# Performance work log

Hardware: AMD Instinct MI355X
Metric: run time of the kernel (lower is better)

## Reference

```python
import jax, jax.numpy as jnp
import numpy as np

N = 100000      # nodes
E = 1600000     # directed edges
F_IN = 128      # node feature dim
H = 128         # hidden dim
C = 16          # classes


def setup_inputs() -> dict:
    key = jax.random.key(0)
    ks = jax.random.split(key, 8)
    s = 1.0 / np.sqrt(H)
    return {
        "x": jax.random.normal(ks[0], (N, F_IN), dtype=jnp.float32),
        "edge_index": jax.random.randint(ks[1], (2, E), 0, N, dtype=jnp.int32),
        "W1": jax.random.normal(ks[2], (F_IN, H), dtype=jnp.float32) * s,
        "b1": jnp.zeros((H,), jnp.float32),
        "W2": jax.random.normal(ks[3], (H, H), dtype=jnp.float32) * s,
        "b2": jnp.zeros((H,), jnp.float32),
        "W3": jax.random.normal(ks[4], (H, H), dtype=jnp.float32) * s,
        "b3": jnp.zeros((H,), jnp.float32),
        "Wfc": jax.random.normal(ks[5], (H, C), dtype=jnp.float32) * s,
        "bfc": jnp.zeros((C,), jnp.float32),
    }


def _gcn_conv(x, W, b, src, dst, norm):
    # x' = b + scatter_add over edges of norm * (x @ W)[src] into dst
    h = x @ W                                   # [N, H] dense GEMM
    msg = h[src] * norm[:, None]                # [E+N, H] gather + scale
    out = jax.ops.segment_sum(msg, dst, num_segments=N)  # scatter-add
    return out + b


def reference(x, edge_index, W1, b1, W2, b2, W3, b3, Wfc, bfc):
    loops = jnp.arange(N, dtype=edge_index.dtype)
    src = jnp.concatenate([edge_index[0], loops])   # [E+N] with self-loops
    dst = jnp.concatenate([edge_index[1], loops])
    # symmetric normalization deg^{-1/2}[src] * deg^{-1/2}[dst] (PyG default)
    deg = jax.ops.segment_sum(jnp.ones_like(dst, dtype=x.dtype), dst, num_segments=N)
    dinv = jax.lax.rsqrt(deg)                       # deg >= 1 due to self-loops
    norm = dinv[src] * dinv[dst]

    h = jax.nn.elu(_gcn_conv(x, W1, b1, src, dst, norm))   # dropout is identity in eval
    h = jax.nn.elu(_gcn_conv(h, W2, b2, src, dst, norm))
    h = jax.nn.elu(_gcn_conv(h, W3, b3, src, dst, norm))
    logits = h @ Wfc + bfc                                  # [N, C]
    return jax.nn.log_softmax(logits, axis=-1)
```

## Files before the change

### kernel.cpp

```cpp
#include <hip/hip_runtime.h>
#include <math.h>

#define HDIM 128
#define CDIM 16
#define CAP 48
#define ASTR 136
#define NBINS 256
#define TILE 4096

typedef unsigned short u16;
typedef unsigned int u32;
typedef __attribute__((ext_vector_type(8))) short short8;
typedef __attribute__((ext_vector_type(4))) float f32x4;

__device__ inline u16 f2bf(float f) {
  u32 u = __float_as_uint(f);
  u += 0x7fffu + ((u >> 16) & 1u);
  return (u16)(u >> 16);
}
__device__ inline float bf_lo(u32 p) { return __uint_as_float(p << 16); }
__device__ inline float bf_hi(u32 p) { return __uint_as_float(p & 0xffff0000u); }
__device__ inline u32 pack2(float a, float b) {
  return (u32)f2bf(a) | ((u32)f2bf(b) << 16);
}
__device__ inline void addp(float2* a, uint4 g) {
  float2 p0 = make_float2(bf_lo(g.x), bf_hi(g.x));
  float2 p1 = make_float2(bf_lo(g.y), bf_hi(g.y));
  float2 p2 = make_float2(bf_lo(g.z), bf_hi(g.z));
  float2 p3 = make_float2(bf_lo(g.w), bf_hi(g.w));
  a[0].x += p0.x; a[0].y += p0.y;
  a[1].x += p1.x; a[1].y += p1.y;
  a[2].x += p2.x; a[2].y += p2.y;
  a[3].x += p3.x; a[3].y += p3.y;
}


__global__ __launch_bounds__(256) void bin_kernel(const int* __restrict__ ei,
                                                  int* __restrict__ cursor,
                                                  int2* __restrict__ bins,
                                                  int binCap, int E, int npb) {
  __shared__ int2 eds[TILE];
  __shared__ int base[NBINS], rank[NBINS], hist[NBINS];
  int tid = threadIdx.x;
  int t0 = blockIdx.x * TILE;
  int n = min(TILE, E - t0);
  for (int i = tid; i < NBINS; i += 256) { hist[i] = 0; rank[i] = 0; }
  __syncthreads();
  for (int i = tid; i < n; i += 256) {
    int s = ei[t0 + i];
    int d = ei[E + t0 + i];
    eds[i] = make_int2(d, s);
    atomicAdd(&hist[d / npb], 1);
  }
  __syncthreads();
  for (int i = tid; i < NBINS; i += 256) {
    int h = hist[i];
    base[i] = h ? atomicAdd(&cursor[i], h) : 0;
  }
  __syncthreads();
  for (int i = tid; i < n; i += 256) {
    int2 e = eds[i];
    int b = e.x / npb;
    int r = base[b] + atomicAdd(&rank[b], 1);
    if (r < binCap) bins[(size_t)b * binCap + r] = e;
  }
}

__global__ __launch_bounds__(256) void fill2_kernel(const int2* __restrict__ bins,
                                                    const int* __restrict__ cursor,
                                                    int binCap, int* __restrict__ deg,
                                                    int* __restrict__ csr,
                                                    float* __restrict__ dinv, int npb, int N) {
  int b = blockIdx.x;
  int cnt = min(cursor[b], binCap);
  const int2* eb = bins + (size_t)b * binCap;
  for (int i = threadIdx.x; i < cnt; i += 256) {
    int2 e = eb[i];
    int p = atomicAdd(&deg[e.x], 1);
    if (p < CAP) csr[(size_t)e.x * CAP + p] = e.y;
  }
  __syncthreads();
  int lo = b * npb, hi = min(lo + npb, N);
  for (int i = lo + threadIdx.x; i < hi; i += 256)
    dinv[i] = rsqrtf((float)(deg[i] + 1));
}


__global__ void prep_kernel(const float* __restrict__ W0, const float* __restrict__ W1,
                            const float* __restrict__ W2, u16* __restrict__ Wt) {
  int t = blockIdx.x * 256 + threadIdx.x;
  int which = t >> 14, idx = t & 16383;
  int n = idx >> 7, k = idx & 127;
  const float* W = which == 0 ? W0 : (which == 1 ? W1 : W2);
  Wt[(size_t)which * HDIM * HDIM + n * HDIM + k] = f2bf(W[k * HDIM + n]);
}


template <bool FP32IN>
__global__ __launch_bounds__(256) void gemm_k(const void* __restrict__ Xv,
                                              const u16* __restrict__ Wt,
                                              const float* __restrict__ dinv,
                                              u16* __restrict__ G, int N) {
  __shared__ u16 As[64 * ASTR];
  __shared__ u16 Wsm[128 * ASTR];
  int tid = threadIdx.x;
  int row0 = blockIdx.x * 64;

  {
    int r = tid >> 2, c = tid & 3;
    int rg = row0 + r;
    if (rg >= N) rg = N - 1;
    uint4* dst = (uint4*)(As + r * ASTR + c * 32);
    if (FP32IN) {
      const float4* src = (const float4*)((const float*)Xv + (size_t)rg * HDIM + c * 32);
#pragma unroll
      for (int j = 0; j < 4; ++j) {
        float4 a = src[2 * j], b = src[2 * j + 1];
        uint4 o;
        o.x = pack2(a.x, a.y); o.y = pack2(a.z, a.w);
        o.z = pack2(b.x, b.y); o.w = pack2(b.z, b.w);
        dst[j] = o;
      }
    } else {
      const uint4* src = (const uint4*)((const u16*)Xv + (size_t)rg * HDIM + c * 32);
      dst[0] = src[0]; dst[1] = src[1]; dst[2] = src[2]; dst[3] = src[3];
    }
  }
  {
    int r = tid >> 1, h = tid & 1;
    const uint4* src = (const uint4*)(Wt + r * HDIM + h * 64);
    uint4* dst = (uint4*)(Wsm + r * ASTR + h * 64);
#pragma unroll
    for (int i = 0; i < 8; ++i) dst[i] = src[i];
  }
  __syncthreads();

  int w = tid >> 6;
  int l = tid & 63;
  int m = l & 15, q = l >> 4;

  f32x4 acc[8];
#pragma unroll
  for (int i = 0; i < 8; ++i) acc[i] = (f32x4){0.f, 0.f, 0.f, 0.f};

#pragma unroll
  for (int kc = 0; kc < 4; ++kc) {
    short8 af = *(const short8*)(As + (w * 16 + m) * ASTR + kc * 32 + q * 8);
#pragma unroll
    for (int nt = 0; nt < 8; ++nt) {
      short8 bfr = *(const short8*)(Wsm + (nt * 16 + m) * ASTR + kc * 32 + q * 8);
      acc[nt] = __builtin_amdgcn_mfma_f32_16x16x32_bf16(af, bfr, acc[nt], 0, 0, 0);
    }
  }
  __syncthreads();

  float dv[4];
#pragma unroll
  for (int r = 0; r < 4; ++r) {
    int rg = row0 + w * 16 + q * 4 + r;
    dv[r] = dinv[rg < N ? rg : N - 1];
  }
#pragma unroll
  for (int nt = 0; nt < 8; ++nt)
#pragma unroll
    for (int r = 0; r < 4; ++r)
      As[(w * 16 + q * 4 + r) * ASTR + nt * 16 + m] = f2bf(acc[nt][r] * dv[r]);
  __syncthreads();

  {
    int r = tid >> 2, c = tid & 3;
    int rg = row0 + r;
    if (rg < N) {
      uint4* dst = (uint4*)(G + (size_t)rg * HDIM + c * 32);
      const uint4* src = (const uint4*)(As + r * ASTR + c * 32);
      dst[0] = src[0]; dst[1] = src[1]; dst[2] = src[2]; dst[3] = src[3];
    }
  }
}


__device__ inline void gather_node(const u16* __restrict__ G, const int* __restrict__ deg,
                                   const int* __restrict__ csr, const float* __restrict__ dinv,
                                   const float4* __restrict__ b4, int node, int l, float* v) {
  float2 a[4];
  {
    uint4 s = *(const uint4*)(G + (size_t)node * HDIM + l * 8);
    a[0] = make_float2(bf_lo(s.x), bf_hi(s.x));
    a[1] = make_float2(bf_lo(s.y), bf_hi(s.y));
    a[2] = make_float2(bf_lo(s.z), bf_hi(s.z));
    a[3] = make_float2(bf_lo(s.w), bf_hi(s.w));
  }
  int d = min(deg[node], CAP);
  const int* row = csr + (size_t)node * CAP;
  int i = 0;
  for (; i + 4 <= d; i += 4) {
    int u0 = row[i], u1 = row[i + 1], u2 = row[i + 2], u3 = row[i + 3];
    uint4 g0 = *(const uint4*)(G + (size_t)u0 * HDIM + l * 8);
    uint4 g1 = *(const uint4*)(G + (size_t)u1 * HDIM + l * 8);
    uint4 g2 = *(const uint4*)(G + (size_t)u2 * HDIM + l * 8);
    uint4 g3 = *(const uint4*)(G + (size_t)u3 * HDIM + l * 8);
    addp(a, g0); addp(a, g1); addp(a, g2); addp(a, g3);
  }
  for (; i < d; ++i) {
    uint4 g = *(const uint4*)(G + (size_t)row[i] * HDIM + l * 8);
    addp(a, g);
  }
  float dvn = dinv[node];
  float4 b0 = b4[l * 2], b1 = b4[l * 2 + 1];
  v[0] = fmaf(dvn, a[0].x, b0.x); v[1] = fmaf(dvn, a[0].y, b0.y);
  v[2] = fmaf(dvn, a[1].x, b0.z); v[3] = fmaf(dvn, a[1].y, b0.w);
  v[4] = fmaf(dvn, a[2].x, b1.x); v[5] = fmaf(dvn, a[2].y, b1.y);
  v[6] = fmaf(dvn, a[3].x, b1.z); v[7] = fmaf(dvn, a[3].y, b1.w);
#pragma unroll
  for (int j = 0; j < 8; ++j) v[j] = v[j] > 0.f ? v[j] : expm1f(v[j]);
}


__global__ __launch_bounds__(256) void agg_bf(const u16* __restrict__ G,
                                              const int* __restrict__ deg,
                                              const int* __restrict__ csr,
                                              const float* __restrict__ dinv,
                                              const float* __restrict__ b,
                                              u16* __restrict__ out, int N) {
  int node = blockIdx.x * 16 + (threadIdx.x >> 4);
  if (node >= N) return;
  int l = threadIdx.x & 15;
  float v[8];
  gather_node(G, deg, csr, dinv, (const float4*)b, node, l, v);
  uint4 o;
  o.x = pack2(v[0], v[1]); o.y = pack2(v[2], v[3]);
  o.z = pack2(v[4], v[5]); o.w = pack2(v[6], v[7]);
  *(uint4*)(out + (size_t)node * HDIM + l * 8) = o;
}


__global__ __launch_bounds__(256) void agg_fc(const u16* __restrict__ G,
                                              const int* __restrict__ deg,
                                              const int* __restrict__ csr,
                                              const float* __restrict__ dinv,
                                              const float* __restrict__ b,
                                              const float* __restrict__ Wfc,
                                              const float* __restrict__ bfc,
                                              float* __restrict__ out, int N) {
  __shared__ u16 As[16 * ASTR];
  __shared__ float Wl[HDIM * CDIM];
  int tid = threadIdx.x;
  for (int i = tid; i < HDIM * CDIM; i += 256) Wl[i] = Wfc[i];

  int node0 = blockIdx.x * 16;
  int lr = tid >> 4, l = tid & 15;
  int node = node0 + lr;
  if (node < N) {
    float v[8];
    gather_node(G, deg, csr, dinv, (const float4*)b, node, l, v);
    uint4 o;
    o.x = pack2(v[0], v[1]); o.y = pack2(v[2], v[3]);
    o.z = pack2(v[4], v[5]); o.w = pack2(v[6], v[7]);
    *(uint4*)(As + lr * ASTR + l * 8) = o;
  }
  __syncthreads();

  int rg = node0 + lr;
  if (rg >= N) return;
  int c = l;
  const u16* hrow = As + lr * ASTR;
  float acc = bfc[c];
#pragma unroll 4
  for (int k8 = 0; k8 < 16; ++k8) {
    uint4 g = *(const uint4*)(hrow + k8 * 8);
    const float* wk = Wl + (k8 * 8) * CDIM + c;
    acc = fmaf(bf_lo(g.x), wk[0 * CDIM], acc);
    acc = fmaf(bf_hi(g.x), wk[1 * CDIM], acc);
    acc = fmaf(bf_lo(g.y), wk[2 * CDIM], acc);
    acc = fmaf(bf_hi(g.y), wk[3 * CDIM], acc);
    acc = fmaf(bf_lo(g.z), wk[4 * CDIM], acc);
    acc = fmaf(bf_hi(g.z), wk[5 * CDIM], acc);
    acc = fmaf(bf_lo(g.w), wk[6 * CDIM], acc);
    acc = fmaf(bf_hi(g.w), wk[7 * CDIM], acc);
  }
  float mx = acc;
  for (int off = 8; off >= 1; off >>= 1) mx = fmaxf(mx, __shfl_xor(mx, off, 16));
  float ex = expf(acc - mx);
  float ssum = ex;
  for (int off = 8; off >= 1; off >>= 1) ssum += __shfl_xor(ssum, off, 16);
  out[(size_t)rg * CDIM + c] = (acc - mx) - logf(ssum);
}


extern "C" void kernel_launch(void* const* d_in, const int* in_sizes, int n_in,
                              void* d_out, int out_size, void* d_ws, size_t ws_size,
                              hipStream_t stream) {
  const float* x   = (const float*)d_in[0];
  const int*   ei  = (const int*)d_in[1];
  const float* W1  = (const float*)d_in[2];
  const float* b1  = (const float*)d_in[3];
  const float* W2  = (const float*)d_in[4];
  const float* b2  = (const float*)d_in[5];
  const float* W3  = (const float*)d_in[6];
  const float* b3  = (const float*)d_in[7];
  const float* Wfc = (const float*)d_in[8];
  const float* bfc = (const float*)d_in[9];

  const int N = in_sizes[0] / HDIM;
  const int E = in_sizes[1] / 2;
  const int npb = (N + NBINS - 1) / NBINS;
  const int binCap = (E + NBINS - 1) / NBINS + 1024;

  char* ws = (char*)d_ws;
  size_t off = 0;
  auto alloc = [&](size_t bytes) -> void* {
    void* p = ws + off;
    off += (bytes + 511) & ~(size_t)511;
    return p;
  };
  size_t degBytes = ((size_t)N * 4 + 511) & ~(size_t)511;
  int*   deg    = (int*)alloc((size_t)N * 4);
  int*   cursor = (int*)alloc((size_t)NBINS * 4);
  float* dinv   = (float*)alloc((size_t)N * 4);
  int*   csr    = (int*)alloc((size_t)N * CAP * 4);
  int2*  bins   = (int2*)alloc((size_t)NBINS * binCap * 8);
  u16*   Wt     = (u16*)alloc((size_t)3 * HDIM * HDIM * 2);
  u16*   A      = (u16*)alloc((size_t)N * HDIM * 2);
  u16*   B      = (u16*)alloc((size_t)N * HDIM * 2);

  hipMemsetAsync(deg, 0, degBytes + 1024, stream);
  bin_kernel<<<(E + TILE - 1) / TILE, 256, 0, stream>>>(ei, cursor, bins, binCap, E, npb);
  fill2_kernel<<<NBINS, 256, 0, stream>>>(bins, cursor, binCap, deg, csr, dinv, npb, N);
  prep_kernel<<<3 * HDIM * HDIM / 256, 256, 0, stream>>>(W1, W2, W3, Wt);

  int grid64 = (N + 63) / 64;
  int grid16 = (N + 15) / 16;
  gemm_k<true><<<grid64, 256, 0, stream>>>(x, Wt, dinv, A, N);
  agg_bf<<<grid16, 256, 0, stream>>>(A, deg, csr, dinv, b1, B, N);
  gemm_k<false><<<grid64, 256, 0, stream>>>(B, Wt + HDIM * HDIM, dinv, A, N);
  agg_bf<<<grid16, 256, 0, stream>>>(A, deg, csr, dinv, b2, B, N);
  gemm_k<false><<<grid64, 256, 0, stream>>>(B, Wt + 2 * HDIM * HDIM, dinv, A, N);
  agg_fc<<<grid16, 256, 0, stream>>>(A, deg, csr, dinv, b3, Wfc, bfc, (float*)d_out, N);
}
```

Before: 420.2 us.

## Fold weight prep and degree zeroing into binning; split CSR fill; compute dinv inline

The weight transpose and bf16 conversion now run as extra blocks of the binning kernel, which also zeroes the degree array, replacing a separate prep launch and a larger memset. The CSR fill kernel is split four ways per bin so more blocks work in parallel. The dinv array is removed and rsqrt(deg+1) is computed where it is used in the GEMM and aggregation kernels. This cuts kernel launches and the serial tail of the fill step, at the cost of a few extra rsqrt ops and relying on the edge blocks covering all N nodes for zeroing deg.

After: 416.2 us. Within noise of the previous version (-0.9%).

```diff
diff --git a/kernel.cpp b/kernel.cpp
--- a/kernel.cpp
+++ b/kernel.cpp
@@ -7,6 +7,7 @@
 #define ASTR 136
 #define NBINS 256
 #define TILE 4096
+#define F2SPLIT 4
 
 typedef unsigned short u16;
 typedef unsigned int u32;
@@ -24,24 +25,37 @@
   return (u32)f2bf(a) | ((u32)f2bf(b) << 16);
 }
 __device__ inline void addp(float2* a, uint4 g) {
-  float2 p0 = make_float2(bf_lo(g.x), bf_hi(g.x));
-  float2 p1 = make_float2(bf_lo(g.y), bf_hi(g.y));
-  float2 p2 = make_float2(bf_lo(g.z), bf_hi(g.z));
-  float2 p3 = make_float2(bf_lo(g.w), bf_hi(g.w));
-  a[0].x += p0.x; a[0].y += p0.y;
-  a[1].x += p1.x; a[1].y += p1.y;
-  a[2].x += p2.x; a[2].y += p2.y;
-  a[3].x += p3.x; a[3].y += p3.y;
+  a[0].x += bf_lo(g.x); a[0].y += bf_hi(g.x);
+  a[1].x += bf_lo(g.y); a[1].y += bf_hi(g.y);
+  a[2].x += bf_lo(g.z); a[2].y += bf_hi(g.z);
+  a[3].x += bf_lo(g.w); a[3].y += bf_hi(g.w);
 }
 
 
 __global__ __launch_bounds__(256) void bin_kernel(const int* __restrict__ ei,
                                                   int* __restrict__ cursor,
                                                   int2* __restrict__ bins,
-                                                  int binCap, int E, int npb) {
+                                                  int binCap, int E, int npb, int nbE,
+                                                  int* __restrict__ deg, int N,
+                                                  const float* __restrict__ W0,
+                                                  const float* __restrict__ W1,
+                                                  const float* __restrict__ W2,
+                                                  u16* __restrict__ Wt) {
+  int tid = threadIdx.x;
+  if (blockIdx.x >= nbE) {
+    int t = (blockIdx.x - nbE) * 256 + tid;
+    int which = t >> 14, idx = t & 16383;
+    int n = idx >> 7, k = idx & 127;
+    const float* W = which == 0 ? W0 : (which == 1 ? W1 : W2);
+    Wt[(size_t)which * HDIM * HDIM + n * HDIM + k] = f2bf(W[k * HDIM + n]);
+    return;
+  }
+  {
+    int i = blockIdx.x * 256 + tid;
+    if (i < N) deg[i] = 0;
+  }
   __shared__ int2 eds[TILE];
   __shared__ int base[NBINS], rank[NBINS], hist[NBINS];
-  int tid = threadIdx.x;
   int t0 = blockIdx.x * TILE;
   int n = min(TILE, E - t0);
   for (int i = tid; i < NBINS; i += 256) { hist[i] = 0; rank[i] = 0; }
@@ -69,37 +83,23 @@
 __global__ __launch_bounds__(256) void fill2_kernel(const int2* __restrict__ bins,
                                                     const int* __restrict__ cursor,
                                                     int binCap, int* __restrict__ deg,
-                                                    int* __restrict__ csr,
-                                                    float* __restrict__ dinv, int npb, int N) {
-  int b = blockIdx.x;
+                                                    int* __restrict__ csr) {
+  int b = blockIdx.x & (NBINS - 1);
+  int part = blockIdx.x >> 8;
   int cnt = min(cursor[b], binCap);
   const int2* eb = bins + (size_t)b * binCap;
-  for (int i = threadIdx.x; i < cnt; i += 256) {
+  for (int i = part * 256 + threadIdx.x; i < cnt; i += 256 * F2SPLIT) {
     int2 e = eb[i];
     int p = atomicAdd(&deg[e.x], 1);
     if (p < CAP) csr[(size_t)e.x * CAP + p] = e.y;
   }
-  __syncthreads();
-  int lo = b * npb, hi = min(lo + npb, N);
-  for (int i = lo + threadIdx.x; i < hi; i += 256)
-    dinv[i] = rsqrtf((float)(deg[i] + 1));
-}
-
-
-__global__ void prep_kernel(const float* __restrict__ W0, const float* __restrict__ W1,
-                            const float* __restrict__ W2, u16* __restrict__ Wt) {
-  int t = blockIdx.x * 256 + threadIdx.x;
-  int which = t >> 14, idx = t & 16383;
-  int n = idx >> 7, k = idx & 127;
-  const float* W = which == 0 ? W0 : (which == 1 ? W1 : W2);
-  Wt[(size_t)which * HDIM * HDIM + n * HDIM + k] = f2bf(W[k * HDIM + n]);
 }
 
 
 template <bool FP32IN>
 __global__ __launch_bounds__(256) void gemm_k(const void* __restrict__ Xv,
                                               const u16* __restrict__ Wt,
-                                              const float* __restrict__ dinv,
+                                              const int* __restrict__ deg,
                                               u16* __restrict__ G, int N) {
   __shared__ u16 As[64 * ASTR];
   __shared__ u16 Wsm[128 * ASTR];
@@ -158,7 +158,7 @@
 #pragma unroll
   for (int r = 0; r < 4; ++r) {
     int rg = row0 + w * 16 + q * 4 + r;
-    dv[r] = dinv[rg < N ? rg : N - 1];
+    dv[r] = rsqrtf((float)(deg[rg < N ? rg : N - 1] + 1));
   }
 #pragma unroll
   for (int nt = 0; nt < 8; ++nt)
@@ -180,7 +180,7 @@
 
 
 __device__ inline void gather_node(const u16* __restrict__ G, const int* __restrict__ deg,
-                                   const int* __restrict__ csr, const float* __restrict__ dinv,
+                                   const int* __restrict__ csr,
                                    const float4* __restrict__ b4, int node, int l, float* v) {
   float2 a[4];
   {
@@ -190,7 +190,8 @@
     a[2] = make_float2(bf_lo(s.z), bf_hi(s.z));
     a[3] = make_float2(bf_lo(s.w), bf_hi(s.w));
   }
-  int d = min(deg[node], CAP);
+  int dfull = deg[node];
+  int d = min(dfull, CAP);
   const int* row = csr + (size_t)node * CAP;
   int i = 0;
   for (; i + 4 <= d; i += 4) {
@@ -205,7 +206,7 @@
     uint4 g = *(const uint4*)(G + (size_t)row[i] * HDIM + l * 8);
     addp(a, g);
   }
-  float dvn = dinv[node];
+  float dvn = rsqrtf((float)(dfull + 1));
   float4 b0 = b4[l * 2], b1 = b4[l * 2 + 1];
   v[0] = fmaf(dvn, a[0].x, b0.x); v[1] = fmaf(dvn, a[0].y, b0.y);
   v[2] = fmaf(dvn, a[1].x, b0.z); v[3] = fmaf(dvn, a[1].y, b0.w);
@@ -219,14 +220,13 @@
 __global__ __launch_bounds__(256) void agg_bf(const u16* __restrict__ G,
                                               const int* __restrict__ deg,
                                               const int* __restrict__ csr,
-                                              const float* __restrict__ dinv,
                                               const float* __restrict__ b,
                                               u16* __restrict__ out, int N) {
   int node = blockIdx.x * 16 + (threadIdx.x >> 4);
   if (node >= N) return;
   int l = threadIdx.x & 15;
   float v[8];
-  gather_node(G, deg, csr, dinv, (const float4*)b, node, l, v);
+  gather_node(G, deg, csr, (const float4*)b, node, l, v);
   uint4 o;
   o.x = pack2(v[0], v[1]); o.y = pack2(v[2], v[3]);
   o.z = pack2(v[4], v[5]); o.w = pack2(v[6], v[7]);
@@ -237,7 +237,6 @@
 __global__ __launch_bounds__(256) void agg_fc(const u16* __restrict__ G,
                                               const int* __restrict__ deg,
                                               const int* __restrict__ csr,
-                                              const float* __restrict__ dinv,
                                               const float* __restrict__ b,
                                               const float* __restrict__ Wfc,
                                               const float* __restrict__ bfc,
@@ -252,7 +251,7 @@
   int node = node0 + lr;
   if (node < N) {
     float v[8];
-    gather_node(G, deg, csr, dinv, (const float4*)b, node, l, v);
+    gather_node(G, deg, csr, (const float4*)b, node, l, v);
     uint4 o;
     o.x = pack2(v[0], v[1]); o.y = pack2(v[2], v[3]);
     o.z = pack2(v[4], v[5]); o.w = pack2(v[6], v[7]);
@@ -305,6 +304,8 @@
   const int E = in_sizes[1] / 2;
   const int npb = (N + NBINS - 1) / NBINS;
   const int binCap = (E + NBINS - 1) / NBINS + 1024;
+  const int nbE = (E + TILE - 1) / TILE;
+  const int nbW = 3 * HDIM * HDIM / 256;
 
   char* ws = (char*)d_ws;
   size_t off = 0;
@@ -313,27 +314,25 @@
     off += (bytes + 511) & ~(size_t)511;
     return p;
   };
-  size_t degBytes = ((size_t)N * 4 + 511) & ~(size_t)511;
   int*   deg    = (int*)alloc((size_t)N * 4);
   int*   cursor = (int*)alloc((size_t)NBINS * 4);
-  float* dinv   = (float*)alloc((size_t)N * 4);
   int*   csr    = (int*)alloc((size_t)N * CAP * 4);
   int2*  bins   = (int2*)alloc((size_t)NBINS * binCap * 8);
   u16*   Wt     = (u16*)alloc((size_t)3 * HDIM * HDIM * 2);
   u16*   A      = (u16*)alloc((size_t)N * HDIM * 2);
   u16*   B      = (u16*)alloc((size_t)N * HDIM * 2);
 
-  hipMemsetAsync(deg, 0, degBytes + 1024, stream);
-  bin_kernel<<<(E + TILE - 1) / TILE, 256, 0, stream>>>(ei, cursor, bins, binCap, E, npb);
-  fill2_kernel<<<NBINS, 256, 0, stream>>>(bins, cursor, binCap, deg, csr, dinv, npb, N);
-  prep_kernel<<<3 * HDIM * HDIM / 256, 256, 0, stream>>>(W1, W2, W3, Wt);
+  hipMemsetAsync(cursor, 0, (size_t)NBINS * 4, stream);
+  bin_kernel<<<nbE + nbW, 256, 0, stream>>>(ei, cursor, bins, binCap, E, npb, nbE, deg, N, W1,
+                                            W2, W3, Wt);
+  fill2_kernel<<<NBINS * F2SPLIT, 256, 0, stream>>>(bins, cursor, binCap, deg, csr);
 
   int grid64 = (N + 63) / 64;
   int grid16 = (N + 15) / 16;
-  gemm_k<true><<<grid64, 256, 0, stream>>>(x, Wt, dinv, A, N);
-  agg_bf<<<grid16, 256, 0, stream>>>(A, deg, csr, dinv, b1, B, N);
-  gemm_k<false><<<grid64, 256, 0, stream>>>(B, Wt + HDIM * HDIM, dinv, A, N);
-  agg_bf<<<grid16, 256, 0, stream>>>(A, deg, csr, dinv, b2, B, N);
-  gemm_k<false><<<grid64, 256, 0, stream>>>(B, Wt + 2 * HDIM * HDIM, dinv, A, N);
-  agg_fc<<<grid16, 256, 0, stream>>>(A, deg, csr, dinv, b3, Wfc, bfc, (float*)d_out, N);
-}
+  gemm_k<true><<<grid64, 256, 0, stream>>>(x, Wt, deg, A, N);
+  agg_bf<<<grid16, 256, 0, stream>>>(A, deg, csr, b1, B, N);
+  gemm_k<false><<<grid64, 256, 0, stream>>>(B, Wt + HDIM * HDIM, deg, A, N);
+  agg_bf<<<grid16, 256, 0, stream>>>(A, deg, csr, b2, B, N);
+  gemm_k<false><<<grid64, 256, 0, stream>>>(B, Wt + 2 * HDIM * HDIM, deg, A, N);
+  agg_fc<<<grid16, 256, 0, stream>>>(A, deg, csr, b3, Wfc, bfc, (float*)d_out, N);
+}
```
